# Performance work log

Measured on AMD Instinct MI355X. Metric: run time of the kernel, lower is better.

Reference implementation:

```python
import jax, jax.numpy as jnp
import numpy as np

B, N, C, H = 16, 577, 768, 12
KEEP_RATE = 0.7


def setup_inputs() -> dict:
    key = jax.random.key(0)
    k1, k2, k3 = jax.random.split(key, 3)
    x = jax.random.normal(k1, (B, N, C), dtype=jnp.float32)
    W_qkv = jax.random.normal(k2, (C, 3 * C), dtype=jnp.float32) * 0.02
    W_proj = jax.random.normal(k3, (C, C), dtype=jnp.float32) * 0.02
    b_proj = jnp.zeros((C,), dtype=jnp.float32)
    return {"x": x, "W_qkv": W_qkv, "W_proj": W_proj, "b_proj": b_proj}


def reference(x, W_qkv, W_proj, b_proj):
    b, n, c = x.shape
    h = H
    dh = c // h
    scale = dh ** (-0.5)

    # qkv projection -> q,k,v each [B,H,N,dh]
    qkv = (x @ W_qkv).reshape(b, n, 3, h, dh)
    qkv = jnp.transpose(qkv, (2, 0, 3, 1, 4))
    q, k, v = qkv[0], qkv[1], qkv[2]

    # full attention scores [B,H,N,N] (materialized, as in the source)
    attn = jnp.einsum('bhnd,bhmd->bhnm', q, k) * scale

    # --- top_pool from row-0 (CLS) scores, attn_method == 'SUM_ABS_1' ---
    # attn[:, :, 0, :] -> [B,H,N]; sum |.| over heads -> [B,N] (== mean over C=1 channel)
    attn_weight = jnp.sum(jnp.abs(attn[:, :, 0, :]), axis=1)  # [B,N]
    # exclude_first=True: drop CLS, topk over remaining N-1, alpha1=1, alpha2=0 (C==1 -> std=0)
    w = attn_weight[:, 1:]                       # [B, N-1]
    keep_num = max(int((n - 1) * KEEP_RATE), 1)  # static
    _, idx = jax.lax.top_k(w, keep_num)          # [B, keep_num]
    idx = jnp.sort(idx, axis=1)
    idx = jnp.concatenate(
        [jnp.zeros((b, 1), dtype=idx.dtype), idx + 1], axis=1)  # prepend CLS index 0
    # expand to [B, keep_num+1, dim] as in torch (pool dim kwarg == self.dim)
    keep_index = jnp.broadcast_to(idx[:, :, None], (b, keep_num + 1, c))

    # standard attention output
    a = jax.nn.softmax(attn, axis=-1)
    out = jnp.einsum('bhnm,bhmd->bhnd', a, v)    # [B,H,N,dh]
    out = jnp.transpose(out, (0, 2, 1, 3)).reshape(b, n, c)
    out = out @ W_proj + b_proj
    return out, keep_index
```

## Files before the change

### kernel.cpp

```cpp
#include <hip/hip_runtime.h>
#include <hip/hip_bf16.h>
#include <stdint.h>

#define B_    16
#define N_    577
#define C_    768
#define H_    12
#define M_    (B_*N_)
#define QKVN  (3*C_)
#define NKEEP 403
#define KROWS (NKEEP+1)
#define VTLD  640
#define PTLD  72

typedef short s16x8 __attribute__((ext_vector_type(8)));
typedef float f32x4 __attribute__((ext_vector_type(4)));

__device__ __forceinline__ unsigned short f2bf(float x){
  unsigned int u = __float_as_uint(x);
  u += 0x7FFF + ((u >> 16) & 1);
  return (unsigned short)(u >> 16);
}

__device__ __forceinline__ void gld_lds16(const void* g, void* l){
  __builtin_amdgcn_global_load_lds(
      (const __attribute__((address_space(1))) unsigned int*)g,
      (__attribute__((address_space(3))) unsigned int*)l, 16, 0, 0);
}

__global__ void k_cvt_x(const float* __restrict__ x, unsigned short* __restrict__ xb){
  int i = blockIdx.x*256 + threadIdx.x;
  float4 v = ((const float4*)x)[i];
  ushort4 o; o.x=f2bf(v.x); o.y=f2bf(v.y); o.z=f2bf(v.z); o.w=f2bf(v.w);
  ((ushort4*)xb)[i] = o;
}

__global__ void k_transpose_cvt(const float* __restrict__ in, unsigned short* __restrict__ out,
                                int R, int CC){
  __shared__ float tile[64][65];
  int r0 = blockIdx.y*64, c0 = blockIdx.x*64;
  int tx = threadIdx.x & 63, ty = threadIdx.x >> 6;
  #pragma unroll
  for(int i=0;i<16;i++){
    int r = ty + i*4;
    tile[r][tx] = in[(size_t)(r0+r)*CC + c0 + tx];
  }
  __syncthreads();
  #pragma unroll
  for(int i=0;i<16;i++){
    int c = ty + i*4;
    out[(size_t)(c0+c)*R + r0 + tx] = f2bf(tile[tx][c]);
  }
}

template<int LDC_, bool BF16OUT>
__global__ __launch_bounds__(256) void k_gemm_bt(const unsigned short* __restrict__ A,
                          const unsigned short* __restrict__ Bt,
                          void* __restrict__ Cout,
                          const float* __restrict__ bias, int Mdim){
  __shared__ __align__(16) unsigned short As[128*32];
  __shared__ __align__(16) unsigned short Bs[128*32];
  const int t = threadIdx.x;
  const int w = t>>6, l = t&63, lq = l>>4, lr = l&15;
  const int wm = w>>1, wn = w&1;
  const int m0 = blockIdx.x*128, n0 = blockIdx.y*128;
  int rA0 = m0 + (t>>2);       if(rA0 >= Mdim) rA0 = Mdim-1;
  int rA1 = m0 + ((t+256)>>2); if(rA1 >= Mdim) rA1 = Mdim-1;
  const unsigned short* gA0 = A  + (size_t)rA0*768 + (t&3)*8;
  const unsigned short* gA1 = A  + (size_t)rA1*768 + (t&3)*8;
  const unsigned short* gB0 = Bt + (size_t)(n0 + (t>>2))*768 + (t&3)*8;
  const unsigned short* gB1 = Bt + (size_t)(n0 + ((t+256)>>2))*768 + (t&3)*8;
  unsigned short* lA0 = As + (size_t)w*512;
  unsigned short* lA1 = As + 2048 + (size_t)w*512;
  unsigned short* lB0 = Bs + (size_t)w*512;
  unsigned short* lB1 = Bs + 2048 + (size_t)w*512;
  f32x4 acc[4][4] = {};
  for(int kt=0; kt<24; ++kt){
    __syncthreads();
    gld_lds16(gA0, lA0); gld_lds16(gA1, lA1);
    gld_lds16(gB0, lB0); gld_lds16(gB1, lB1);
    gA0 += 32; gA1 += 32; gB0 += 32; gB1 += 32;
    __syncthreads();
    s16x8 af[4], bfr[4];
    #pragma unroll
    for(int it=0;it<4;it++) af[it]  = *(const s16x8*)&As[(wm*64+it*16+lr)*32 + lq*8];
    #pragma unroll
    for(int jt=0;jt<4;jt++) bfr[jt] = *(const s16x8*)&Bs[(wn*64+jt*16+lr)*32 + lq*8];
    #pragma unroll
    for(int it=0;it<4;it++)
      #pragma unroll
      for(int jt=0;jt<4;jt++)
        acc[it][jt] = __builtin_amdgcn_mfma_f32_16x16x32_bf16(af[it], bfr[jt], acc[it][jt], 0,0,0);
  }
  #pragma unroll
  for(int it=0;it<4;it++){
    #pragma unroll
    for(int r=0;r<4;r++){
      int row = m0 + wm*64 + it*16 + lq*4 + r;
      if(row < Mdim){
        #pragma unroll
        for(int jt=0;jt<4;jt++){
          int col = n0 + wn*64 + jt*16 + lr;
          float v = acc[it][jt][r];
          if constexpr (BF16OUT)
            ((unsigned short*)Cout)[(size_t)row*LDC_ + col] = f2bf(v);
          else
            ((float*)Cout)[(size_t)row*LDC_ + col] = v + bias[col];
        }
      }
    }
  }
}

__global__ void k_transpose_v(const unsigned short* __restrict__ qkv,
                              unsigned short* __restrict__ vtbuf){
  __shared__ __align__(16) unsigned short tile[64*80];
  const int bh = blockIdx.x, b = bh/12, h = bh%12;
  const int n0 = blockIdx.y*64;
  const int t = threadIdx.x;
  const size_t vbase = (size_t)(b*577)*2304 + 1536 + h*64;
  #pragma unroll
  for(int i=0;i<2;i++){
    int task = t + i*256;
    int row = task>>3, c = task&7;
    int n = n0 + row; if(n > 576) n = 576;
    *(uint4*)&tile[row*80 + c*8] = *(const uint4*)&qkv[vbase + (size_t)n*2304 + c*8];
  }
  __syncthreads();
  #pragma unroll
  for(int i=0;i<2;i++){
    int task = t + i*256;
    int d = task&63, nc = task>>6;
    unsigned short v[8];
    #pragma unroll
    for(int e=0;e<8;e++) v[e] = tile[(nc*8+e)*80 + d];
    *(uint4*)&vtbuf[(size_t)(bh*64+d)*VTLD + n0 + nc*8] = *(uint4*)v;
  }
}

__global__ __launch_bounds__(256,4) void k_attn(const unsigned short* __restrict__ qkv,
                                                const unsigned short* __restrict__ vtbuf,
                                                unsigned short* __restrict__ aout){
  __shared__ __align__(16) unsigned short Ks[64*64];
  __shared__ __align__(16) unsigned short Vt[64*64];
  __shared__ __align__(16) unsigned short Ptt[128*PTLD];
  __shared__ float Ls[4][2][16][4];
  const int blk = blockIdx.x;
  const int bh = blk % 192, qt = blk / 192;
  const int b = bh / 12, h = bh % 12;
  const int t = threadIdx.x, w = t>>6, l = t&63, lq = l>>4, lr = l&15;
  const size_t base = (size_t)(b*577)*2304 + h*64;
  const int q0 = qt*128;
  s16x8 bq[2][2];
  #pragma unroll
  for(int it=0;it<2;it++){
    int qrow = q0 + w*32 + it*16 + lr; if(qrow > 576) qrow = 576;
    #pragma unroll
    for(int ks=0;ks<2;ks++)
      bq[it][ks] = *(const s16x8*)&qkv[base + (size_t)qrow*2304 + ks*32 + lq*8];
  }
  const int srow = w*8 + (l>>3);
  const int cswz8 = (((l&7) ^ (l>>3)) << 3);
  unsigned short* ldsK = Ks + (size_t)w*512;
  unsigned short* ldsV = Vt + (size_t)w*512;
  const unsigned short* gVbase = vtbuf + (size_t)(bh*64)*VTLD + cswz8;

  f32x4 acc_o[2][4] = {};
  float lsum[2] = {0.f, 0.f};
  const float CEXP = 0.18033688011112043f;

  for(int j0=0; j0<577; j0+=64){
    __syncthreads();
    #pragma unroll
    for(int i=0;i<2;i++){
      int krow = j0 + i*32 + srow; if(krow > 576) krow = 576;
      gld_lds16(qkv + base + 768 + (size_t)krow*2304 + cswz8, ldsK + i*2048);
      gld_lds16(gVbase + (size_t)(i*32 + srow)*VTLD + j0,     ldsV + i*2048);
    }
    __syncthreads();
    f32x4 accs[2][4] = {};
    #pragma unroll
    for(int ks=0;ks<2;ks++){
      s16x8 ak[4];
      #pragma unroll
      for(int jt=0;jt<4;jt++){
        int j = jt*16 + lr;
        ak[jt] = *(const s16x8*)&Ks[j*64 + (((4*ks+lq) ^ (j&7))<<3)];
      }
      #pragma unroll
      for(int it=0;it<2;it++)
        #pragma unroll
        for(int jt=0;jt<4;jt++)
          accs[it][jt] = __builtin_amdgcn_mfma_f32_16x16x32_bf16(ak[jt], bq[it][ks], accs[it][jt], 0,0,0);
    }
    #pragma unroll
    for(int it=0;it<2;it++){
      int qlocal = w*32 + it*16 + lr;
      #pragma unroll
      for(int jt=0;jt<4;jt++){
        ushort4 pk;
        unsigned short* pks = (unsigned short*)&pk;
        #pragma unroll
        for(int r=0;r<4;r++){
          int j = j0 + jt*16 + lq*4 + r;
          float p = exp2f(accs[it][jt][r] * CEXP);
          if(j > 576) p = 0.f;
          lsum[it] += p;
          pks[r] = f2bf(p);
        }
        *(ushort4*)&Ptt[qlocal*PTLD + jt*16 + lq*4] = pk;
      }
    }
    #pragma unroll
    for(int ks=0;ks<2;ks++){
      s16x8 ap[2], bv[4];
      #pragma unroll
      for(int it=0;it<2;it++)
        ap[it] = *(const s16x8*)&Ptt[(w*32+it*16+lr)*PTLD + ks*32 + lq*8];
      #pragma unroll
      for(int dt=0;dt<4;dt++){
        int d = dt*16 + lr;
        bv[dt] = *(const s16x8*)&Vt[d*64 + (((4*ks+lq) ^ (d&7))<<3)];
      }
      #pragma unroll
      for(int it=0;it<2;it++)
        #pragma unroll
        for(int dt=0;dt<4;dt++)
          acc_o[it][dt] = __builtin_amdgcn_mfma_f32_16x16x32_bf16(ap[it], bv[dt], acc_o[it][dt], 0,0,0);
    }
  }
  #pragma unroll
  for(int it=0;it<2;it++) Ls[w][it][lr][lq] = lsum[it];
  #pragma unroll
  for(int it=0;it<2;it++){
    #pragma unroll
    for(int r=0;r<4;r++){
      int n = q0 + w*32 + it*16 + lq*4 + r;
      if(n <= 576){
        int q16 = lq*4 + r;
        float lt = Ls[w][it][q16][0] + Ls[w][it][q16][1] + Ls[w][it][q16][2] + Ls[w][it][q16][3];
        float inv = 1.f / lt;
        #pragma unroll
        for(int dt=0;dt<4;dt++)
          aout[(size_t)(b*577+n)*768 + h*64 + dt*16 + lr] = f2bf(acc_o[it][dt][r]*inv);
      }
    }
  }
}

__global__ void k_qcls(const float* __restrict__ x, const float* __restrict__ Wqkv,
                       float* __restrict__ qcls){
  __shared__ float xs[768];
  __shared__ float part[4][64];
  const int b = blockIdx.y, j0 = blockIdx.x*64;
  const int t = threadIdx.x;
  const float* xr = x + (size_t)b*577*768;
  xs[t] = xr[t]; xs[t+256] = xr[t+256]; xs[t+512] = xr[t+512];
  __syncthreads();
  const int jl = t & 63, cs = t >> 6;
  float acc = 0.f;
  const float* wp = Wqkv + (size_t)(cs*192)*2304 + j0 + jl;
  #pragma unroll 4
  for(int c=0;c<192;c++){ acc += xs[cs*192+c] * wp[0]; wp += 2304; }
  part[cs][jl] = acc;
  __syncthreads();
  if(t < 64) qcls[b*768 + j0 + t] = part[0][t]+part[1][t]+part[2][t]+part[3][t];
}
__global__ void k_u(const float* __restrict__ Wqkv, const float* __restrict__ qcls,
                    float* __restrict__ u){
  int h = blockIdx.x, b = blockIdx.y, c = threadIdx.x;
  const float* qc = qcls + b*768 + h*64;
  const float* wr = Wqkv + (size_t)c*2304 + 768 + h*64;
  float acc = 0.f;
  #pragma unroll
  for(int d=0;d<64;d++) acc += wr[d]*qc[d];
  u[(size_t)(b*12+h)*768 + c] = acc;
}
__global__ void k_attw(const float* __restrict__ x, const float* __restrict__ u,
                       float* __restrict__ attw){
  int blk = blockIdx.x;
  int b = blk/577, m = blk%577;
  int lane = threadIdx.x;
  const float* xr = x + (size_t)(b*577+m)*768;
  const float* ub = u + (size_t)b*12*768;
  float part[12];
  #pragma unroll
  for(int h=0;h<12;h++) part[h]=0.f;
  #pragma unroll
  for(int i=0;i<12;i++){
    float xv = xr[i*64 + lane];
    #pragma unroll
    for(int h=0;h<12;h++) part[h] += xv * ub[h*768 + i*64 + lane];
  }
  float s = 0.f;
  #pragma unroll
  for(int h=0;h<12;h++){
    float v = part[h];
    #pragma unroll
    for(int off=32; off; off>>=1) v += __shfl_xor(v, off);
    s += fabsf(v);
  }
  if(lane==0) attw[b*577 + m] = 0.125f * s;
}
__global__ void k_topk(const float* __restrict__ attw, int* __restrict__ idxbuf){
  __shared__ float sw[576];
  __shared__ int wtot[9];
  int b = blockIdx.x, t = threadIdx.x;
  float wv = attw[b*577 + 1 + t];
  sw[t] = wv;
  __syncthreads();
  int rank = 0;
  for(int j=0;j<576;j++){
    float wj = sw[j];
    rank += (wj > wv) || (wj == wv && j < t);
  }
  bool kept = rank < NKEEP;
  unsigned long long mask = __ballot(kept);
  int wid = t>>6, lane = t&63;
  int pos = __popcll(mask & ((1ull<<lane)-1ull));
  if(lane==0) wtot[wid] = __popcll(mask);
  __syncthreads();
  int off0 = 0;
  for(int q=0;q<wid;q++) off0 += wtot[q];
  if(kept) idxbuf[b*KROWS + 1 + off0 + pos] = t+1;
  if(t==0) idxbuf[b*KROWS] = 0;
}
__global__ void k_fill_keep(const int* __restrict__ idxbuf, float* __restrict__ out2){
  int i4 = blockIdx.x*256 + threadIdx.x;
  float v = (float)idxbuf[i4/192];
  ((float4*)out2)[i4] = make_float4(v,v,v,v);
}

extern "C" void kernel_launch(void* const* d_in, const int* in_sizes, int n_in,
                              void* d_out, int out_size, void* d_ws, size_t ws_size,
                              hipStream_t stream){
  const float* x     = (const float*)d_in[0];
  const float* Wqkv  = (const float*)d_in[1];
  const float* Wproj = (const float*)d_in[2];
  const float* bias  = (const float*)d_in[3];
  float* out  = (float*)d_out;
  float* out2 = out + (size_t)M_*768;

  char* ws = (char*)d_ws;
  size_t off = 0;
  auto alloc = [&](size_t bytes)->void*{ void* p = ws + off; off += (bytes + 255) & ~(size_t)255; return p; };
  unsigned short* xb     = (unsigned short*)alloc((size_t)M_*768*2);
  unsigned short* wqkvT  = (unsigned short*)alloc((size_t)QKVN*768*2);
  unsigned short* wprojT = (unsigned short*)alloc((size_t)768*768*2);
  unsigned short* qkvb   = (unsigned short*)alloc((size_t)M_*QKVN*2);
  unsigned short* aoutb  = (unsigned short*)alloc((size_t)M_*768*2);
  unsigned short* vtbuf  = (unsigned short*)alloc((size_t)192*64*VTLD*2);
  float* qcls   = (float*)alloc((size_t)16*768*4);
  float* u      = (float*)alloc((size_t)16*12*768*4);
  float* attw   = (float*)alloc((size_t)16*577*4);
  int*   idxbuf = (int*)alloc((size_t)16*KROWS*4);

  k_cvt_x<<<6924, 256, 0, stream>>>(x, xb);
  k_transpose_cvt<<<dim3(36,12), 256, 0, stream>>>(Wqkv,  wqkvT, 768, 2304);
  k_transpose_cvt<<<dim3(12,12), 256, 0, stream>>>(Wproj, wprojT, 768, 768);
  k_gemm_bt<QKVN, true><<<dim3(73,18), 256, 0, stream>>>(xb, wqkvT, qkvb, nullptr, M_);
  k_qcls<<<dim3(12,16), 256, 0, stream>>>(x, Wqkv, qcls);
  k_u<<<dim3(12,16), 768, 0, stream>>>(Wqkv, qcls, u);
  k_attw<<<16*577, 64, 0, stream>>>(x, u, attw);
  k_topk<<<16, 576, 0, stream>>>(attw, idxbuf);
  k_fill_keep<<<(16*KROWS*768/4 + 255)/256, 256, 0, stream>>>(idxbuf, out2);
  k_transpose_v<<<dim3(192,10), 256, 0, stream>>>(qkvb, vtbuf);
  k_attn<<<960, 256, 0, stream>>>(qkvb, vtbuf, aoutb);
  k_gemm_bt<768, false><<<dim3(73,6), 256, 0, stream>>>(aoutb, wprojT, out, bias, M_);
}
```

Before: 302.2 us.

## Fuse V transpose into QKV GEMM epilogue, remap tiles, restructure CLS-score kernels

The QKV GEMM epilogue now writes V tiles directly in transposed layout into the V-transpose buffer, which removes the separate k_transpose_v kernel and its read-back of V. A 1D grid with an XCD-aware tile mapping groups M tiles per chiplet so that L2 reuse improves. The qcls, u and attw kernels are rewritten to stage operands in shared memory and handle several batches or rows per block, cutting redundant global reads and the tiny 64-thread blocks. The transposed V stores are 8-byte strided writes, which may be less coalesced than the old tiled transpose.

```diff
diff --git a/kernel.cpp b/kernel.cpp
--- a/kernel.cpp
+++ b/kernel.cpp
@@ -28,6 +28,21 @@
       (__attribute__((address_space(3))) unsigned int*)l, 16, 0, 0);
 }
 
+template<int NT>
+__device__ __forceinline__ void tile_map(int L, int& mt, int& nt){
+  constexpr int NB = 73*NT;
+  int x = L & 7, j = L >> 3;
+  if(j < 9*NT){
+    nt = j/9; mt = x*9 + (j - nt*9);
+  } else {
+    mt = 72;
+    int offt = 0;
+    #pragma unroll
+    for(int y=0;y<8;y++) if(y<x) offt += ((NB-1-y)>>3) + 1 - 9*NT;
+    nt = offt + (j - 9*NT);
+  }
+}
+
 __global__ void k_cvt_x(const float* __restrict__ x, unsigned short* __restrict__ xb){
   int i = blockIdx.x*256 + threadIdx.x;
   float4 v = ((const float4*)x)[i];
@@ -53,17 +68,19 @@
   }
 }
 
-template<int LDC_, bool BF16OUT>
+template<int LDC_, bool BF16OUT, bool FUSEV, int NT>
 __global__ __launch_bounds__(256) void k_gemm_bt(const unsigned short* __restrict__ A,
                           const unsigned short* __restrict__ Bt,
                           void* __restrict__ Cout,
-                          const float* __restrict__ bias, int Mdim){
+                          const float* __restrict__ bias, int Mdim,
+                          unsigned short* __restrict__ vtbuf){
   __shared__ __align__(16) unsigned short As[128*32];
   __shared__ __align__(16) unsigned short Bs[128*32];
   const int t = threadIdx.x;
   const int w = t>>6, l = t&63, lq = l>>4, lr = l&15;
   const int wm = w>>1, wn = w&1;
-  const int m0 = blockIdx.x*128, n0 = blockIdx.y*128;
+  int mt, nt; tile_map<NT>(blockIdx.x, mt, nt);
+  const int m0 = mt*128, n0 = nt*128;
   int rA0 = m0 + (t>>2);       if(rA0 >= Mdim) rA0 = Mdim-1;
   int rA1 = m0 + ((t+256)>>2); if(rA1 >= Mdim) rA1 = Mdim-1;
   const unsigned short* gA0 = A  + (size_t)rA0*768 + (t&3)*8;
@@ -92,49 +109,50 @@
       for(int jt=0;jt<4;jt++)
         acc[it][jt] = __builtin_amdgcn_mfma_f32_16x16x32_bf16(af[it], bfr[jt], acc[it][jt], 0,0,0);
   }
-  #pragma unroll
-  for(int it=0;it<4;it++){
-    #pragma unroll
-    for(int r=0;r<4;r++){
-      int row = m0 + wm*64 + it*16 + lq*4 + r;
-      if(row < Mdim){
+  if(FUSEV && n0 >= 1536){
+    #pragma unroll
+    for(int it=0;it<4;it++){
+      int tok0 = m0 + wm*64 + it*16 + lq*4;
+      #pragma unroll
+      for(int jt=0;jt<4;jt++){
+        int vrow = (n0 - 1536) + wn*64 + jt*16 + lr;
+        ushort4 pk; unsigned short* pks = (unsigned short*)&pk;
         #pragma unroll
-        for(int jt=0;jt<4;jt++){
-          int col = n0 + wn*64 + jt*16 + lr;
-          float v = acc[it][jt][r];
-          if constexpr (BF16OUT)
-            ((unsigned short*)Cout)[(size_t)row*LDC_ + col] = f2bf(v);
-          else
-            ((float*)Cout)[(size_t)row*LDC_ + col] = v + bias[col];
+        for(int r=0;r<4;r++) pks[r] = f2bf(acc[it][jt][r]);
+        int b0 = tok0/577, t0 = tok0 - b0*577;
+        if(tok0 + 3 < M_ && t0 + 3 < 577){
+          *(ushort4*)&vtbuf[(size_t)(b0*768 + vrow)*VTLD + t0] = pk;
+        } else {
+          #pragma unroll
+          for(int r=0;r<4;r++){
+            int tg = tok0 + r;
+            if(tg < M_){
+              int bb = tg/577, tt = tg - bb*577;
+              vtbuf[(size_t)(bb*768 + vrow)*VTLD + tt] = pks[r];
+            }
+          }
         }
       }
     }
-  }
-}
-
-__global__ void k_transpose_v(const unsigned short* __restrict__ qkv,
-                              unsigned short* __restrict__ vtbuf){
-  __shared__ __align__(16) unsigned short tile[64*80];
-  const int bh = blockIdx.x, b = bh/12, h = bh%12;
-  const int n0 = blockIdx.y*64;
-  const int t = threadIdx.x;
-  const size_t vbase = (size_t)(b*577)*2304 + 1536 + h*64;
-  #pragma unroll
-  for(int i=0;i<2;i++){
-    int task = t + i*256;
-    int row = task>>3, c = task&7;
-    int n = n0 + row; if(n > 576) n = 576;
-    *(uint4*)&tile[row*80 + c*8] = *(const uint4*)&qkv[vbase + (size_t)n*2304 + c*8];
-  }
-  __syncthreads();
-  #pragma unroll
-  for(int i=0;i<2;i++){
-    int task = t + i*256;
-    int d = task&63, nc = task>>6;
-    unsigned short v[8];
-    #pragma unroll
-    for(int e=0;e<8;e++) v[e] = tile[(nc*8+e)*80 + d];
-    *(uint4*)&vtbuf[(size_t)(bh*64+d)*VTLD + n0 + nc*8] = *(uint4*)v;
+  } else {
+    #pragma unroll
+    for(int it=0;it<4;it++){
+      #pragma unroll
+      for(int r=0;r<4;r++){
+        int row = m0 + wm*64 + it*16 + lq*4 + r;
+        if(row < Mdim){
+          #pragma unroll
+          for(int jt=0;jt<4;jt++){
+            int col = n0 + wn*64 + jt*16 + lr;
+            float v = acc[it][jt][r];
+            if constexpr (BF16OUT)
+              ((unsigned short*)Cout)[(size_t)row*LDC_ + col] = f2bf(v);
+            else
+              ((float*)Cout)[(size_t)row*LDC_ + col] = v + bias[col];
+          }
+        }
+      }
+    }
   }
 }
 
@@ -250,57 +268,86 @@
 
 __global__ void k_qcls(const float* __restrict__ x, const float* __restrict__ Wqkv,
                        float* __restrict__ qcls){
-  __shared__ float xs[768];
-  __shared__ float part[4][64];
-  const int b = blockIdx.y, j0 = blockIdx.x*64;
+  __shared__ float xs[16*768];
+  const int j0 = blockIdx.x*32;
   const int t = threadIdx.x;
-  const float* xr = x + (size_t)b*577*768;
-  xs[t] = xr[t]; xs[t+256] = xr[t+256]; xs[t+512] = xr[t+512];
-  __syncthreads();
-  const int jl = t & 63, cs = t >> 6;
-  float acc = 0.f;
-  const float* wp = Wqkv + (size_t)(cs*192)*2304 + j0 + jl;
-  #pragma unroll 4
-  for(int c=0;c<192;c++){ acc += xs[cs*192+c] * wp[0]; wp += 2304; }
-  part[cs][jl] = acc;
-  __syncthreads();
-  if(t < 64) qcls[b*768 + j0 + t] = part[0][t]+part[1][t]+part[2][t]+part[3][t];
+  #pragma unroll
+  for(int i=0;i<12;i++){
+    int idx = t + i*256;
+    int b = idx/192, k4 = idx - b*192;
+    ((float4*)xs)[b*192 + k4] = ((const float4*)(x + (size_t)b*577*768))[k4];
+  }
+  __syncthreads();
+  const int jl = t & 31, bg = t >> 5;
+  #pragma unroll
+  for(int p=0;p<2;p++){
+    int b = p*8 + bg;
+    float acc = 0.f;
+    const float* wp = Wqkv + j0 + jl;
+    #pragma unroll 4
+    for(int c=0;c<768;c++){ acc += xs[b*768 + c] * wp[0]; wp += 2304; }
+    qcls[b*768 + j0 + jl] = acc;
+  }
 }
 __global__ void k_u(const float* __restrict__ Wqkv, const float* __restrict__ qcls,
                     float* __restrict__ u){
-  int h = blockIdx.x, b = blockIdx.y, c = threadIdx.x;
-  const float* qc = qcls + b*768 + h*64;
-  const float* wr = Wqkv + (size_t)c*2304 + 768 + h*64;
-  float acc = 0.f;
-  #pragma unroll
-  for(int d=0;d<64;d++) acc += wr[d]*qc[d];
-  u[(size_t)(b*12+h)*768 + c] = acc;
+  __shared__ float Wl[64*65];
+  __shared__ float qc[16*64];
+  const int c0 = blockIdx.x*64, h = blockIdx.y;
+  const int t = threadIdx.x;
+  #pragma unroll
+  for(int i=0;i<4;i++){
+    int idx = t + i*256;
+    int cl = idx >> 4, c4 = idx & 15;
+    float4 v = *(const float4*)&Wqkv[(size_t)(c0+cl)*2304 + 768 + h*64 + c4*4];
+    Wl[cl*65 + c4*4+0] = v.x; Wl[cl*65 + c4*4+1] = v.y;
+    Wl[cl*65 + c4*4+2] = v.z; Wl[cl*65 + c4*4+3] = v.w;
+  }
+  { int b = t >> 4, d4 = t & 15;
+    *(float4*)&qc[b*64 + d4*4] = *(const float4*)&qcls[b*768 + h*64 + d4*4]; }
+  __syncthreads();
+  const int cl = t & 63, bg = t >> 6;
+  #pragma unroll
+  for(int p=0;p<4;p++){
+    int b = p*4 + bg;
+    float acc = 0.f;
+    #pragma unroll
+    for(int d=0;d<64;d++) acc += Wl[cl*65 + d] * qc[b*64 + d];
+    u[(size_t)(b*12+h)*768 + c0 + cl] = acc;
+  }
 }
 __global__ void k_attw(const float* __restrict__ x, const float* __restrict__ u,
                        float* __restrict__ attw){
-  int blk = blockIdx.x;
-  int b = blk/577, m = blk%577;
-  int lane = threadIdx.x;
-  const float* xr = x + (size_t)(b*577+m)*768;
-  const float* ub = u + (size_t)b*12*768;
-  float part[12];
-  #pragma unroll
-  for(int h=0;h<12;h++) part[h]=0.f;
-  #pragma unroll
-  for(int i=0;i<12;i++){
-    float xv = xr[i*64 + lane];
-    #pragma unroll
-    for(int h=0;h<12;h++) part[h] += xv * ub[h*768 + i*64 + lane];
-  }
-  float s = 0.f;
-  #pragma unroll
-  for(int h=0;h<12;h++){
-    float v = part[h];
-    #pragma unroll
-    for(int off=32; off; off>>=1) v += __shfl_xor(v, off);
-    s += fabsf(v);
-  }
-  if(lane==0) attw[b*577 + m] = 0.125f * s;
+  __shared__ float us[12*768];
+  __shared__ float part[4][64];
+  const int rt = blockIdx.x, b = blockIdx.y;
+  const int t = threadIdx.x;
+  #pragma unroll
+  for(int i=0;i<9;i++)
+    ((float4*)us)[t + i*256] = ((const float4*)(u + (size_t)b*12*768))[t + i*256];
+  __syncthreads();
+  const int rl = t & 63, hg = t >> 6;
+  int r = rt*64 + rl; int rc = r > 576 ? 576 : r;
+  const float4* xr = (const float4*)(x + (size_t)(b*577+rc)*768);
+  const float* u0 = us + (hg*3+0)*768;
+  const float* u1 = us + (hg*3+1)*768;
+  const float* u2 = us + (hg*3+2)*768;
+  float a0=0.f, a1=0.f, a2=0.f;
+  #pragma unroll 4
+  for(int k4=0;k4<192;k4++){
+    float4 xv = xr[k4];
+    int k = k4*4;
+    a0 += xv.x*u0[k] + xv.y*u0[k+1] + xv.z*u0[k+2] + xv.w*u0[k+3];
+    a1 += xv.x*u1[k] + xv.y*u1[k+1] + xv.z*u1[k+2] + xv.w*u1[k+3];
+    a2 += xv.x*u2[k] + xv.y*u2[k+1] + xv.z*u2[k+2] + xv.w*u2[k+3];
+  }
+  part[hg][rl] = fabsf(a0) + fabsf(a1) + fabsf(a2);
+  __syncthreads();
+  if(t < 64){
+    int rr = rt*64 + t;
+    if(rr <= 576)
+      attw[b*577 + rr] = 0.125f*(part[0][t]+part[1][t]+part[2][t]+part[3][t]);
+  }
 }
 __global__ void k_topk(const float* __restrict__ attw, int* __restrict__ idxbuf){
   __shared__ float sw[576];
@@ -358,13 +405,12 @@
   k_cvt_x<<<6924, 256, 0, stream>>>(x, xb);
   k_transpose_cvt<<<dim3(36,12), 256, 0, stream>>>(Wqkv,  wqkvT, 768, 2304);
   k_transpose_cvt<<<dim3(12,12), 256, 0, stream>>>(Wproj, wprojT, 768, 768);
-  k_gemm_bt<QKVN, true><<<dim3(73,18), 256, 0, stream>>>(xb, wqkvT, qkvb, nullptr, M_);
-  k_qcls<<<dim3(12,16), 256, 0, stream>>>(x, Wqkv, qcls);
-  k_u<<<dim3(12,16), 768, 0, stream>>>(Wqkv, qcls, u);
-  k_attw<<<16*577, 64, 0, stream>>>(x, u, attw);
+  k_gemm_bt<QKVN, true, true, 18><<<73*18, 256, 0, stream>>>(xb, wqkvT, qkvb, nullptr, M_, vtbuf);
+  k_qcls<<<24, 256, 0, stream>>>(x, Wqkv, qcls);
+  k_u<<<dim3(12,12), 256, 0, stream>>>(Wqkv, qcls, u);
+  k_attw<<<dim3(10,16), 256, 0, stream>>>(x, u, attw);
   k_topk<<<16, 576, 0, stream>>>(attw, idxbuf);
   k_fill_keep<<<(16*KROWS*768/4 + 255)/256, 256, 0, stream>>>(idxbuf, out2);
-  k_transpose_v<<<dim3(192,10), 256, 0, stream>>>(qkvb, vtbuf);
   k_attn<<<960, 256, 0, stream>>>(qkvb, vtbuf, aoutb);
-  k_gemm_bt<768, false><<<dim3(73,6), 256, 0, stream>>>(aoutb, wprojT, out, bias, M_);
-}
+  k_gemm_bt<768, false, false, 6><<<73*6, 256, 0, stream>>>(aoutb, wprojT, out, bias, M_, nullptr);
+}
```

Result: slower. 369.1 us (+22.1%).
